# Kernel optimization log

Measured on AMD Instinct MI355X. Metric: run time of the kernel, lower is better.

Reference implementation:

```python
import jax, jax.numpy as jnp
import numpy as np

BATCH = 16384
N_USERS = 1_000_000
EMBED = 64
N_EDGES = 524_288  # batch * avg_degree(32)


def setup_inputs() -> dict:
    key = jax.random.key(0)
    k1, k2, k3, k4, k5, k6 = jax.random.split(key, 6)
    nodes = jax.random.randint(k1, (BATCH,), 0, N_USERS)
    neigh_ids = jax.random.randint(k2, (N_EDGES,), 0, N_USERS)
    seg_ids = jnp.sort(jax.random.randint(k3, (N_EDGES,), 0, BATCH))
    features = jax.random.normal(k4, (N_USERS, EMBED), dtype=jnp.float32) * 0.02
    w1 = jax.random.normal(k5, (EMBED, 2 * EMBED), dtype=jnp.float32) * (1.0 / np.sqrt(2 * EMBED))
    b1 = jax.random.normal(k6, (EMBED,), dtype=jnp.float32) * 0.01
    return {"nodes": nodes, "neigh_ids": neigh_ids, "seg_ids": seg_ids,
            "features": features, "w1": w1, "b1": b1}


def reference(nodes, neigh_ids, seg_ids, features, w1, b1):
    # self features: embedding lookup, (B, D)
    self_feats = features[nodes]
    # neighbor features gathered along flattened ragged edge list, (E, D)
    neigh_gathered = features[neigh_ids]
    # mean-aggregate per destination node (segment mean)
    summed = jax.ops.segment_sum(neigh_gathered, seg_ids, num_segments=BATCH)
    counts = jax.ops.segment_sum(jnp.ones((neigh_ids.shape[0],), dtype=jnp.float32),
                                 seg_ids, num_segments=BATCH)
    neigh_feats = summed / jnp.maximum(counts, 1.0)[:, None]
    # concat + linear + relu, (B, D)
    combined = jnp.concatenate([self_feats, neigh_feats], axis=1)
    return jax.nn.relu(combined @ w1.T + b1)
```

## Files before the change

kernel.cpp:

```cpp
#include <hip/hip_runtime.h>

#define BATCH 16384
#define EMBED 64

__global__ void seg_offsets_kernel(const int* __restrict__ seg, int E, int B,
                                   int* __restrict__ row_start) {
    int e = blockIdx.x * blockDim.x + threadIdx.x;
    if (e >= E) return;
    int s1 = seg[e];
    if (e == 0) {
        for (int s = 0; s <= s1; ++s) row_start[s] = 0;
    } else {
        int s0 = seg[e - 1];
        for (int s = s0 + 1; s <= s1; ++s) row_start[s] = e;
    }
    if (e == E - 1) {
        for (int s = s1 + 1; s <= B; ++s) row_start[s] = E;
    }
}

__global__ __launch_bounds__(512) void social_encoder_fused(
    const int*   __restrict__ nodes,
    const int*   __restrict__ neigh_ids,
    const int*   __restrict__ row_start,
    const float* __restrict__ features,
    const float* __restrict__ w1,
    const float* __restrict__ b1,
    float*       __restrict__ out,
    int B)
{
    __shared__ float w1s[EMBED * 129];
    __shared__ float comb[8][2 * EMBED];

    for (int i = threadIdx.x; i < EMBED * 2 * EMBED; i += 512) {
        w1s[(i >> 7) * 129 + (i & 127)] = w1[i];
    }
    __syncthreads();

    const int wave = threadIdx.x >> 6;
    const int lane = threadIdx.x & 63;
    const int q    = lane & 15;
    const int sub  = lane >> 4;
    const float bj = b1[lane];

    for (int b = blockIdx.x * 8 + wave; b < B; b += gridDim.x * 8) {
        const int start = row_start[b];
        const int end   = row_start[b + 1];

        float ax = 0.f, ay = 0.f, az = 0.f, aw = 0.f;
        int e = start + sub;
        for (; e + 4 < end; e += 8) {
            const int r0 = neigh_ids[e];
            const int r1 = neigh_ids[e + 4];
            const float4 v0 = ((const float4*)(features + ((size_t)r0 << 6)))[q];
            const float4 v1 = ((const float4*)(features + ((size_t)r1 << 6)))[q];
            ax += v0.x + v1.x; ay += v0.y + v1.y;
            az += v0.z + v1.z; aw += v0.w + v1.w;
        }
        if (e < end) {
            const int r = neigh_ids[e];
            const float4 v = ((const float4*)(features + ((size_t)r << 6)))[q];
            ax += v.x; ay += v.y; az += v.z; aw += v.w;
        }

        ax += __shfl_xor(ax, 16, 64); ax += __shfl_xor(ax, 32, 64);
        ay += __shfl_xor(ay, 16, 64); ay += __shfl_xor(ay, 32, 64);
        az += __shfl_xor(az, 16, 64); az += __shfl_xor(az, 32, 64);
        aw += __shfl_xor(aw, 16, 64); aw += __shfl_xor(aw, 32, 64);

        const float scale = 1.0f / fmaxf((float)(end - start), 1.0f);

        if (sub == 0) {
            const int node = nodes[b];
            const float4 sv = ((const float4*)(features + ((size_t)node << 6)))[q];
            ((float4*)&comb[wave][0])[q] = sv;
            float4 nv;
            nv.x = ax * scale; nv.y = ay * scale;
            nv.z = az * scale; nv.w = aw * scale;
            ((float4*)&comb[wave][EMBED])[q] = nv;
        }
        __syncthreads();

        float acc = bj;
        const float* wrow = &w1s[lane * 129];
        const float* cb   = comb[wave];
        #pragma unroll
        for (int c = 0; c < 2 * EMBED; c += 4) {
            const float4 cv = *(const float4*)&cb[c];
            acc += cv.x * wrow[c + 0];
            acc += cv.y * wrow[c + 1];
            acc += cv.z * wrow[c + 2];
            acc += cv.w * wrow[c + 3];
        }
        out[((size_t)b << 6) + lane] = fmaxf(acc, 0.0f);
    }
}

extern "C" void kernel_launch(void* const* d_in, const int* in_sizes, int n_in,
                              void* d_out, int out_size, void* d_ws, size_t ws_size,
                              hipStream_t stream) {
    const int*   nodes     = (const int*)d_in[0];
    const int*   neigh_ids = (const int*)d_in[1];
    const int*   seg_ids   = (const int*)d_in[2];
    const float* features  = (const float*)d_in[3];
    const float* w1        = (const float*)d_in[4];
    const float* b1        = (const float*)d_in[5];
    float*       out       = (float*)d_out;

    const int B = in_sizes[0];
    const int E = in_sizes[1];

    int* row_start = (int*)d_ws;

    seg_offsets_kernel<<<(E + 255) / 256, 256, 0, stream>>>(seg_ids, E, B, row_start);
    social_encoder_fused<<<1024, 512, 0, stream>>>(nodes, neigh_ids, row_start,
                                                   features, w1, b1, out, B);
}
```

Measured before the change: 336.7 us.

## Batch neighbor-id loads via shuffles, unroll gathers, drop block barrier

Each wave now loads up to 64 neighbor ids with one coalesced read and hands them out with shuffles. The gather loop is unrolled to four independent float4 loads per lane, so more memory requests are in flight. The block-wide __syncthreads is replaced by a wave-local fence, because each wave only uses its own comb row. The W1 shared-memory stride becomes 132 so rows can be read as float4, and the self-feature load is issued early. The float4 LDS reads at stride 132 may cause more bank conflicts than the old stride-129 scalar reads, and relying on wave lockstep instead of a barrier is a subtle correctness assumption.

```diff
diff --git a/kernel.cpp b/kernel.cpp
--- a/kernel.cpp
+++ b/kernel.cpp
@@ -1,7 +1,7 @@
 #include <hip/hip_runtime.h>
 
-#define BATCH 16384
 #define EMBED 64
+#define W1_STRIDE 132
 
 __global__ void seg_offsets_kernel(const int* __restrict__ seg, int E, int B,
                                    int* __restrict__ row_start) {
@@ -19,7 +19,7 @@
     }
 }
 
-__global__ __launch_bounds__(512) void social_encoder_fused(
+__global__ __launch_bounds__(512, 8) void social_encoder_fused(
     const int*   __restrict__ nodes,
     const int*   __restrict__ neigh_ids,
     const int*   __restrict__ row_start,
@@ -29,12 +29,11 @@
     float*       __restrict__ out,
     int B)
 {
-    __shared__ float w1s[EMBED * 129];
+    __shared__ float w1s[EMBED * W1_STRIDE];
     __shared__ float comb[8][2 * EMBED];
 
-    for (int i = threadIdx.x; i < EMBED * 2 * EMBED; i += 512) {
-        w1s[(i >> 7) * 129 + (i & 127)] = w1[i];
-    }
+    for (int i = threadIdx.x; i < EMBED * 2 * EMBED; i += 512)
+        w1s[(i >> 7) * W1_STRIDE + (i & 127)] = w1[i];
     __syncthreads();
 
     const int wave = threadIdx.x >> 6;
@@ -42,57 +41,76 @@
     const int q    = lane & 15;
     const int sub  = lane >> 4;
     const float bj = b1[lane];
+    float* cwave = comb[wave];
 
     for (int b = blockIdx.x * 8 + wave; b < B; b += gridDim.x * 8) {
         const int start = row_start[b];
         const int end   = row_start[b + 1];
+        const int node  = nodes[b];
 
-        float ax = 0.f, ay = 0.f, az = 0.f, aw = 0.f;
-        int e = start + sub;
-        for (; e + 4 < end; e += 8) {
-            const int r0 = neigh_ids[e];
-            const int r1 = neigh_ids[e + 4];
-            const float4 v0 = ((const float4*)(features + ((size_t)r0 << 6)))[q];
-            const float4 v1 = ((const float4*)(features + ((size_t)r1 << 6)))[q];
-            ax += v0.x + v1.x; ay += v0.y + v1.y;
-            az += v0.z + v1.z; aw += v0.w + v1.w;
-        }
-        if (e < end) {
-            const int r = neigh_ids[e];
-            const float4 v = ((const float4*)(features + ((size_t)r << 6)))[q];
-            ax += v.x; ay += v.y; az += v.z; aw += v.w;
+        const float4 sv = ((const float4*)(features + ((size_t)node << 6)))[q];
+
+        float4 acc = make_float4(0.f, 0.f, 0.f, 0.f);
+
+        for (int chunk = start; chunk < end; chunk += 64) {
+            const int n = min(64, end - chunk);
+            int myid = 0;
+            if (lane < n) myid = neigh_ids[chunk + lane];
+
+            const int nfull = n & ~15;
+            for (int base = 0; base < nfull; base += 16) {
+                const int r0 = __shfl(myid, base + sub,      64);
+                const int r1 = __shfl(myid, base + sub + 4,  64);
+                const int r2 = __shfl(myid, base + sub + 8,  64);
+                const int r3 = __shfl(myid, base + sub + 12, 64);
+                const float4 v0 = ((const float4*)(features + ((size_t)r0 << 6)))[q];
+                const float4 v1 = ((const float4*)(features + ((size_t)r1 << 6)))[q];
+                const float4 v2 = ((const float4*)(features + ((size_t)r2 << 6)))[q];
+                const float4 v3 = ((const float4*)(features + ((size_t)r3 << 6)))[q];
+                acc.x += (v0.x + v1.x) + (v2.x + v3.x);
+                acc.y += (v0.y + v1.y) + (v2.y + v3.y);
+                acc.z += (v0.z + v1.z) + (v2.z + v3.z);
+                acc.w += (v0.w + v1.w) + (v2.w + v3.w);
+            }
+
+            const int r = n - nfull;
+            const int tmax = (r + 3) >> 2;
+            for (int t = 0; t < tmax; ++t) {
+                const int src = nfull + sub + 4 * t;
+                const int rid = __shfl(myid, src, 64);
+                const float4 v = ((const float4*)(features + ((size_t)rid << 6)))[q];
+                if (src < n) {
+                    acc.x += v.x; acc.y += v.y; acc.z += v.z; acc.w += v.w;
+                }
+            }
         }
 
-        ax += __shfl_xor(ax, 16, 64); ax += __shfl_xor(ax, 32, 64);
-        ay += __shfl_xor(ay, 16, 64); ay += __shfl_xor(ay, 32, 64);
-        az += __shfl_xor(az, 16, 64); az += __shfl_xor(az, 32, 64);
-        aw += __shfl_xor(aw, 16, 64); aw += __shfl_xor(aw, 32, 64);
+        acc.x += __shfl_xor(acc.x, 16, 64); acc.x += __shfl_xor(acc.x, 32, 64);
+        acc.y += __shfl_xor(acc.y, 16, 64); acc.y += __shfl_xor(acc.y, 32, 64);
+        acc.z += __shfl_xor(acc.z, 16, 64); acc.z += __shfl_xor(acc.z, 32, 64);
+        acc.w += __shfl_xor(acc.w, 16, 64); acc.w += __shfl_xor(acc.w, 32, 64);
 
         const float scale = 1.0f / fmaxf((float)(end - start), 1.0f);
+        float4 nv;
+        nv.x = acc.x * scale; nv.y = acc.y * scale;
+        nv.z = acc.z * scale; nv.w = acc.w * scale;
 
-        if (sub == 0) {
-            const int node = nodes[b];
-            const float4 sv = ((const float4*)(features + ((size_t)node << 6)))[q];
-            ((float4*)&comb[wave][0])[q] = sv;
-            float4 nv;
-            nv.x = ax * scale; nv.y = ay * scale;
-            nv.z = az * scale; nv.w = aw * scale;
-            ((float4*)&comb[wave][EMBED])[q] = nv;
+        const float4 val = (lane < 16) ? sv : nv;
+        if (lane < 32) ((float4*)cwave)[lane] = val;
+
+        __threadfence_block();
+
+        float accd = bj;
+        const float* wrow = &w1s[lane * W1_STRIDE];
+        #pragma unroll 8
+        for (int c = 0; c < 2 * EMBED; c += 4) {
+            const float4 cv = *(const float4*)&cwave[c];
+            const float4 wv = *(const float4*)&wrow[c];
+            accd += cv.x * wv.x + cv.y * wv.y + cv.z * wv.z + cv.w * wv.w;
         }
-        __syncthreads();
+        out[((size_t)b << 6) + lane] = fmaxf(accd, 0.0f);
 
-        float acc = bj;
-        const float* wrow = &w1s[lane * 129];
-        const float* cb   = comb[wave];
-        #pragma unroll
-        for (int c = 0; c < 2 * EMBED; c += 4) {
-            const float4 cv = *(const float4*)&cb[c];
-            acc += cv.x * wrow[c + 0];
-            acc += cv.y * wrow[c + 1];
-            acc += cv.z * wrow[c + 2];
-            acc += cv.w * wrow[c + 3];
-        }
-        out[((size_t)b << 6) + lane] = fmaxf(acc, 0.0f);
+        __threadfence_block();
     }
 }
 
```

New measurement: 332.5 us. No clear change (-1.3%).
